# Kernel tuning notes

Measured on AMD Instinct MI355X. Metric: run time of the kernel, lower is better.

## Reference

```python
import jax, jax.numpy as jnp
import numpy as np

C = 1024
HEADS = 8
HD = C // HEADS
SF = 2
EPS = 1e-6
N, D, H, W = 2, 32, 40, 32


def _ln(x, w, b):
    m = jnp.mean(x, -1, keepdims=True)
    v = jnp.mean((x - m) ** 2, -1, keepdims=True)
    return (x - m) * jax.lax.rsqrt(v + EPS) * w + b


def _mlp2(x, w1, b1, w2, b2):
    # Linear -> exact GELU -> Linear (matches nn.Sequential(Linear, GELU, Linear))
    return jax.nn.gelu(x @ w1.T + b1, approximate=False) @ w2.T + b2


def setup_inputs() -> dict:
    key = jax.random.key(0)
    ks = jax.random.split(key, 24)
    p = lambda i, shape: jax.random.normal(ks[i], shape, jnp.float32) * 0.02
    return {
        "x": jax.random.normal(ks[0], (N, D, H, W, C), jnp.float32),
        "q_w": p(1, (C, C)),
        "k_w1": p(2, (C, C)), "k_b1": p(3, (C,)),
        "k_w2": p(4, (C, C)), "k_b2": p(5, (C,)),
        "v_w1": p(6, (C, C)), "v_b1": p(7, (C,)),
        "v_w2": p(8, (C, C)), "v_b2": p(9, (C,)),
        "lnq_w": jnp.ones((C,), jnp.float32), "lnq_b": jnp.zeros((C,), jnp.float32),
        "lnk_w": jnp.ones((C,), jnp.float32), "lnk_b": jnp.zeros((C,), jnp.float32),
        "lnv_w": jnp.ones((C,), jnp.float32), "lnv_b": jnp.zeros((C,), jnp.float32),
        "in_w": p(10, (3 * C, C)), "in_b": p(11, (3 * C,)),
        "out_w": p(12, (C, C)), "out_b": p(13, (C,)),
        "mlp_w1": p(14, (2 * C, C)), "mlp_b1": p(15, (2 * C,)),
        "mlp_w2": p(16, (2 * C, 2 * C)), "mlp_b2": p(17, (2 * C,)),
    }


def reference(x, q_w, k_w1, k_b1, k_w2, k_b2, v_w1, v_b1, v_w2, v_b2,
              lnq_w, lnq_b, lnk_w, lnk_b, lnv_w, lnv_b,
              in_w, in_b, out_w, out_b, mlp_w1, mlp_b1, mlp_w2, mlp_b2):
    n, d, h, w, c = x.shape
    dg, hg, wg = d // SF, h // SF, w // SF
    cube = SF ** 3

    x_flat = x.reshape(n, -1, c)                      # [N, T, C], T = D*H*W
    k = _ln(_mlp2(x_flat, k_w1, k_b1, k_w2, k_b2), lnk_w, lnk_b)
    v = _ln(_mlp2(x_flat, v_w1, v_b1, v_w2, v_b2), lnv_w, lnv_b)

    # Trilinear downsample by exactly 2 (align_corners=False) == 2x2x2 mean pool.
    q = x.reshape(n, dg, SF, hg, SF, wg, SF, c).mean(axis=(2, 4, 6))
    q = q.reshape(n, -1, c)                            # [N, Q, C]
    query = _ln(q @ q_w.T, lnq_w, lnq_b)               # q_proj_1 has no bias

    def regions(t):
        t = t.reshape(n, dg, SF, hg, SF, wg, SF, c)
        t = t.transpose(0, 1, 3, 5, 2, 4, 6, 7)
        return t.reshape(n, dg * hg * wg, cube, c)     # [N, Q, 8, C]

    k_r = regions(k)
    v_r = regions(v)

    wq, wk, wv = in_w[:C], in_w[C:2 * C], in_w[2 * C:]
    bq, bk, bv = in_b[:C], in_b[C:2 * C], in_b[2 * C:]
    qh = (query @ wq.T + bq).reshape(n, -1, HEADS, HD)           # [N,Q,h,hd]
    kh = (k_r @ wk.T + bk).reshape(n, -1, cube, HEADS, HD)       # [N,Q,8,h,hd]
    vh = (v_r @ wv.T + bv).reshape(n, -1, cube, HEADS, HD)

    scale = 1.0 / np.sqrt(HD).astype(np.float32)
    scores = jnp.einsum('nqhd,nqkhd->nqhk', qh, kh) * scale
    attn = jax.nn.softmax(scores, axis=-1)
    o = jnp.einsum('nqhk,nqkhd->nqhd', attn, vh).reshape(n, -1, c)
    o = o @ out_w.T + out_b                            # MHA out_proj

    o = _mlp2(o, mlp_w1, mlp_b1, mlp_w2, mlp_b2)       # [N, Q, 2C]
    return o.reshape(n, dg, hg, wg, 2 * c)
```

## Files before the change

kernel.cpp:

```cpp
#include <hip/hip_runtime.h>

typedef __attribute__((ext_vector_type(8))) short bf16x8;
typedef __attribute__((ext_vector_type(4))) float f32x4;
typedef unsigned short u16;

__device__ inline u16 f2b(float f) {
  union { float f; unsigned u; } x; x.f = f;
  unsigned r = x.u + 0x7FFFu + ((x.u >> 16) & 1u);
  return (u16)(r >> 16);
}
__device__ inline float b2f(u16 s) {
  union { unsigned u; float f; } x; x.u = ((unsigned)s) << 16;
  return x.f;
}
__device__ inline float gelu_f(float v) {
  return 0.5f * v * (1.0f + erff(v * 0.70710678118654752f));
}
__device__ inline void gll16(const void* g, void* lds) {
  __builtin_amdgcn_global_load_lds((const __attribute__((address_space(1))) void*)g,
                                   (__attribute__((address_space(3))) void*)lds,
                                   16, 0, 0);
}

__global__ __launch_bounds__(256) void cvt_w(const float* __restrict__ s,
                                             u16* __restrict__ d, int n4) {
  int i = blockIdx.x * 256 + threadIdx.x;
  if (i < n4) {
    float4 v = ((const float4*)s)[i];
    ushort4 o; o.x = f2b(v.x); o.y = f2b(v.y); o.z = f2b(v.z); o.w = f2b(v.w);
    ((ushort4*)d)[i] = o;
  }
}

__global__ __launch_bounds__(256) void pool_cvt(const float* __restrict__ xg,
                                                u16* __restrict__ Xb,
                                                u16* __restrict__ Qp) {
  int qr = blockIdx.x;
  int wgi = qr & 15;
  int hgi = (qr >> 4) % 20;
  int dgi = qr / 320;
  int c = threadIdx.x * 4;
  float sx = 0.f, sy = 0.f, sz = 0.f, sw = 0.f;
#pragma unroll
  for (int j = 0; j < 8; ++j) {
    int tr = ((2 * dgi + (j >> 2)) * 40 + (2 * hgi + ((j >> 1) & 1))) * 32 +
             (2 * wgi + (j & 1));
    long off = (long)tr * 1024 + c;
    float4 v = *(const float4*)&xg[off];
    ushort4 o; o.x = f2b(v.x); o.y = f2b(v.y); o.z = f2b(v.z); o.w = f2b(v.w);
    *(ushort4*)&Xb[off] = o;
    sx += v.x; sy += v.y; sz += v.z; sw += v.w;
  }
  ushort4 o;
  o.x = f2b(sx * 0.125f); o.y = f2b(sy * 0.125f);
  o.z = f2b(sz * 0.125f); o.w = f2b(sw * 0.125f);
  *(ushort4*)&Qp[(long)qr * 1024 + c] = o;
}

__global__ __launch_bounds__(256) void ln_ip(u16* __restrict__ X,
                                             const float* __restrict__ w,
                                             const float* __restrict__ b) {
  long row = blockIdx.x;
  int c = threadIdx.x * 4;
  ushort4 v = *(const ushort4*)&X[row * 1024 + c];
  float f0 = b2f(v.x), f1 = b2f(v.y), f2 = b2f(v.z), f3 = b2f(v.w);
  float s = f0 + f1 + f2 + f3;
  float q = f0 * f0 + f1 * f1 + f2 * f2 + f3 * f3;
#pragma unroll
  for (int off = 32; off >= 1; off >>= 1) {
    s += __shfl_xor(s, off);
    q += __shfl_xor(q, off);
  }
  __shared__ float red[8];
  int wv = threadIdx.x >> 6, ln = threadIdx.x & 63;
  if (ln == 0) { red[wv] = s; red[4 + wv] = q; }
  __syncthreads();
  s = red[0] + red[1] + red[2] + red[3];
  q = red[4] + red[5] + red[6] + red[7];
  float mean = s * (1.f / 1024.f);
  float var = q * (1.f / 1024.f) - mean * mean;
  float rs = rsqrtf(var + 1e-6f);
  float4 wv4 = *(const float4*)&w[c];
  float4 bv4 = *(const float4*)&b[c];
  ushort4 o;
  o.x = f2b((f0 - mean) * rs * wv4.x + bv4.x);
  o.y = f2b((f1 - mean) * rs * wv4.y + bv4.y);
  o.z = f2b((f2 - mean) * rs * wv4.z + bv4.z);
  o.w = f2b((f3 - mean) * rs * wv4.w + bv4.w);
  *(ushort4*)&X[row * 1024 + c] = o;
}

#define TM 128
#define TN 128
#define TK 32
template <int EPI>
__global__ __launch_bounds__(256) void gemm_bt(const u16* __restrict__ A,
                                               const u16* __restrict__ B,
                                               const float* __restrict__ bias,
                                               float* __restrict__ Cf,
                                               u16* __restrict__ Cb,
                                               int M, int N, int K) {
  __shared__ __align__(16) u16 As[TM * TK];
  __shared__ __align__(16) u16 Bs[TN * TK];
  const int tid = threadIdx.x;
  const int l = tid & 63;
  const int wv = tid >> 6;
  const int wm = (wv >> 1) * 64, wn = (wv & 1) * 64;
  const int bm = blockIdx.x * TM, bn = blockIdx.y * TN;
  const int lr = l & 15, kg = l >> 4;

  f32x4 acc[4][4] = {};

  for (int k0 = 0; k0 < K; k0 += TK) {
#pragma unroll
    for (int i = 0; i < 2; ++i) {
      int e = (i * 256 + tid) * 8;
      int r = e >> 5, c = e & 31;
      int ga = bm + r; if (ga > M - 1) ga = M - 1;
      gll16(A + (long)ga * K + k0 + c, As + e);
      int gb = bn + r;
      gll16(B + (long)gb * K + k0 + c, Bs + e);
    }
    __syncthreads();
    bf16x8 af[4], bfr[4];
#pragma unroll
    for (int m = 0; m < 4; ++m)
      af[m] = *(const bf16x8*)&As[(wm + m * 16 + lr) * TK + kg * 8];
#pragma unroll
    for (int n = 0; n < 4; ++n)
      bfr[n] = *(const bf16x8*)&Bs[(wn + n * 16 + lr) * TK + kg * 8];
#pragma unroll
    for (int m = 0; m < 4; ++m)
#pragma unroll
      for (int n = 0; n < 4; ++n)
        acc[m][n] = __builtin_amdgcn_mfma_f32_16x16x32_bf16(af[m], bfr[n],
                                                            acc[m][n], 0, 0, 0);
    __syncthreads();
  }

#pragma unroll
  for (int m = 0; m < 4; ++m) {
    int row0 = bm + wm + m * 16 + kg * 4;
#pragma unroll
    for (int n = 0; n < 4; ++n) {
      int col = bn + wn + n * 16 + lr;
      float bsv = (EPI == 3) ? 0.f : bias[col];
#pragma unroll
      for (int r = 0; r < 4; ++r) {
        int row = row0 + r;
        if (row < M) {
          float v = acc[m][n][r] + bsv;
          if (EPI == 1) v = gelu_f(v);
          if (EPI == 2) Cf[(long)row * N + col] = v;
          else Cb[(long)row * N + col] = f2b(v);
        }
      }
    }
  }
}

__global__ __launch_bounds__(256) void attn_k(const u16* __restrict__ QH,
                                              const u16* __restrict__ KH,
                                              const u16* __restrict__ VH,
                                              u16* __restrict__ O, int dgc) {
  int qr = blockIdx.x;
  int wgi = qr & 15;
  int hgi = (qr >> 4) % 20;
  int dgi = qr / 320;
  int c0 = (threadIdx.x >> 5) * 128 + (threadIdx.x & 31) * 4;
  ushort4 qv = *(const ushort4*)&QH[(long)qr * 1024 + c0];
  float q0 = b2f(qv.x), q1 = b2f(qv.y), q2 = b2f(qv.z), q3 = b2f(qv.w);
  long trs[8];
  float sc[8];
#pragma unroll
  for (int j = 0; j < 8; ++j) {
    int tr = ((2 * dgi + (j >> 2)) * 40 + (2 * hgi + ((j >> 1) & 1))) * 32 +
             (2 * wgi + (j & 1));
    trs[j] = (long)tr * 1024 + c0;
    ushort4 kv = *(const ushort4*)&KH[trs[j]];
    float p = q0 * b2f(kv.x) + q1 * b2f(kv.y) + q2 * b2f(kv.z) + q3 * b2f(kv.w);
    p += __shfl_xor(p, 16); p += __shfl_xor(p, 8); p += __shfl_xor(p, 4);
    p += __shfl_xor(p, 2);  p += __shfl_xor(p, 1);
    sc[j] = p * 0.088388347648318447f;
  }
  float mx = sc[0];
#pragma unroll
  for (int j = 1; j < 8; ++j) mx = fmaxf(mx, sc[j]);
  float ssum = 0.f;
#pragma unroll
  for (int j = 0; j < 8; ++j) { sc[j] = expf(sc[j] - mx); ssum += sc[j]; }
  float inv = 1.0f / ssum;
  float o0 = 0, o1 = 0, o2 = 0, o3 = 0;
#pragma unroll
  for (int j = 0; j < 8; ++j) {
    ushort4 vv = *(const ushort4*)&VH[trs[j]];
    float p = sc[j] * inv;
    o0 += p * b2f(vv.x); o1 += p * b2f(vv.y);
    o2 += p * b2f(vv.z); o3 += p * b2f(vv.w);
  }
  ushort4 ov; ov.x = f2b(o0); ov.y = f2b(o1); ov.z = f2b(o2); ov.w = f2b(o3);
  *(ushort4*)&O[(long)qr * 1024 + c0] = ov;
}

extern "C" void kernel_launch(void* const* d_in, const int* in_sizes, int n_in,
                              void* d_out, int out_size, void* d_ws,
                              size_t ws_size, hipStream_t stream) {
  const float* x      = (const float*)d_in[0];
  const float* q_w    = (const float*)d_in[1];
  const float* k_w1   = (const float*)d_in[2];
  const float* k_b1   = (const float*)d_in[3];
  const float* k_w2   = (const float*)d_in[4];
  const float* k_b2   = (const float*)d_in[5];
  const float* v_w1   = (const float*)d_in[6];
  const float* v_b1   = (const float*)d_in[7];
  const float* v_w2   = (const float*)d_in[8];
  const float* v_b2   = (const float*)d_in[9];
  const float* lnq_w  = (const float*)d_in[10];
  const float* lnq_b  = (const float*)d_in[11];
  const float* lnk_w  = (const float*)d_in[12];
  const float* lnk_b  = (const float*)d_in[13];
  const float* lnv_w  = (const float*)d_in[14];
  const float* lnv_b  = (const float*)d_in[15];
  const float* in_w   = (const float*)d_in[16];
  const float* in_b   = (const float*)d_in[17];
  const float* out_w  = (const float*)d_in[18];
  const float* out_b  = (const float*)d_in[19];
  const float* mlp_w1 = (const float*)d_in[20];
  const float* mlp_b1 = (const float*)d_in[21];
  const float* mlp_w2 = (const float*)d_in[22];
  const float* mlp_b2 = (const float*)d_in[23];
  float* out = (float*)d_out;

  char* base = (char*)d_ws;
  size_t off = 0;
  auto alloc_us = [&](size_t elems) -> u16* {
    u16* r = (u16*)(base + off);
    off += ((elems * 2 + 255) & ~(size_t)255);
    return r;
  };
  const size_t CC = 1024 * 1024;
  u16* wb_q   = alloc_us(CC);
  u16* wb_k1  = alloc_us(CC);
  u16* wb_k2  = alloc_us(CC);
  u16* wb_v1  = alloc_us(CC);
  u16* wb_v2  = alloc_us(CC);
  u16* wb_in  = alloc_us(3 * CC);
  u16* wb_out = alloc_us(CC);
  u16* wb_m1  = alloc_us(2 * CC);
  u16* wb_m2  = alloc_us(4 * CC);

  auto cvt = [&](const float* s, u16* d, size_t n) {
    int n4 = (int)(n / 4);
    cvt_w<<<(n4 + 255) / 256, 256, 0, stream>>>(s, d, n4);
  };
  cvt(q_w, wb_q, CC);     cvt(k_w1, wb_k1, CC);  cvt(k_w2, wb_k2, CC);
  cvt(v_w1, wb_v1, CC);   cvt(v_w2, wb_v2, CC);  cvt(in_w, wb_in, 3 * CC);
  cvt(out_w, wb_out, CC); cvt(mlp_w1, wb_m1, 2 * CC); cvt(mlp_w2, wb_m2, 4 * CC);

  int s = 16;
  for (int cand = 1; cand <= 16; cand <<= 1) {
    size_t Tc_ = 40960ull / cand;
    size_t need = off + Tc_ * 9472ull + (1ull << 20);
    if (need <= ws_size) { s = cand; break; }
  }
  const int dcount = 32 / s;
  const int dgc = dcount / 2;
  const int Tc = dcount * 1280;
  const int Tq = dgc * 320;

  u16* Xb  = alloc_us((size_t)Tc * 1024);
  u16* Hb  = alloc_us((size_t)Tc * 1024);
  u16* Kb  = alloc_us((size_t)Tc * 1024);
  u16* Vb  = alloc_us((size_t)Tc * 1024);
  u16* Qp  = alloc_us((size_t)Tq * 1024);
  u16* QQ  = alloc_us((size_t)Tq * 1024);
  u16* QHb = alloc_us((size_t)Tq * 1024);
  u16* Ob  = alloc_us((size_t)Tq * 1024);
  u16* O2  = alloc_us((size_t)Tq * 1024);
  u16* Hm  = Xb;

  dim3 gBig((Tc + 127) / 128, 1024 / 128);
  dim3 gSm((Tq + 127) / 128, 1024 / 128);
  dim3 gM1((Tq + 127) / 128, 2048 / 128);

  for (int n = 0; n < 2; ++n) {
    for (int sl = 0; sl < s; ++sl) {
      long tok0 = (long)n * 40960 + (long)sl * dcount * 1280;
      long q0g  = (long)n * 5120 + (long)sl * dgc * 320;
      const float* xg = x + tok0 * 1024;

      pool_cvt<<<Tq, 256, 0, stream>>>(xg, Xb, Qp);

      gemm_bt<1><<<gBig, 256, 0, stream>>>(Xb, wb_k1, k_b1, nullptr, Hb, Tc, 1024, 1024);
      gemm_bt<0><<<gBig, 256, 0, stream>>>(Hb, wb_k2, k_b2, nullptr, Kb, Tc, 1024, 1024);
      ln_ip<<<Tc, 256, 0, stream>>>(Kb, lnk_w, lnk_b);

      gemm_bt<1><<<gBig, 256, 0, stream>>>(Xb, wb_v1, v_b1, nullptr, Hb, Tc, 1024, 1024);
      gemm_bt<0><<<gBig, 256, 0, stream>>>(Hb, wb_v2, v_b2, nullptr, Vb, Tc, 1024, 1024);
      ln_ip<<<Tc, 256, 0, stream>>>(Vb, lnv_w, lnv_b);

      gemm_bt<3><<<gSm, 256, 0, stream>>>(Qp, wb_q, nullptr, nullptr, QQ, Tq, 1024, 1024);
      ln_ip<<<Tq, 256, 0, stream>>>(QQ, lnq_w, lnq_b);
      gemm_bt<0><<<gSm, 256, 0, stream>>>(QQ, wb_in, in_b, nullptr, QHb, Tq, 1024, 1024);

      gemm_bt<0><<<gBig, 256, 0, stream>>>(Kb, wb_in + CC, in_b + 1024, nullptr, Hb, Tc, 1024, 1024);
      gemm_bt<0><<<gBig, 256, 0, stream>>>(Vb, wb_in + 2 * CC, in_b + 2048, nullptr, Xb, Tc, 1024, 1024);

      attn_k<<<Tq, 256, 0, stream>>>(QHb, Hb, Xb, Ob, dgc);

      gemm_bt<0><<<gSm, 256, 0, stream>>>(Ob, wb_out, out_b, nullptr, O2, Tq, 1024, 1024);
      gemm_bt<1><<<gM1, 256, 0, stream>>>(O2, wb_m1, mlp_b1, nullptr, Hm, Tq, 2048, 1024);
      gemm_bt<2><<<gM1, 256, 0, stream>>>(Hm, wb_m2, mlp_b2, out + q0g * 2048, nullptr, Tq, 2048, 2048);
    }
  }
}
```

Baseline: 2.686 ms.

## Double-buffer GEMM LDS tiles, fuse K/V first MLP layers, add XCD-aware block swizzle

The GEMM kernel now uses two LDS buffers so the next K-tile loads while the current one is computed, halving the number of barriers per tile. The K and V first MLP layers are merged into one N=2048 GEMM over concatenated weights and biases, and the second layers read strided halves through a new lda parameter. Blocks are launched on a 1D grid and remapped so each XCD gets contiguous M-tiles, meant to improve L2 reuse. The trade-off is double the LDS per block, which may lower occupancy, plus a larger hidden buffer that can force more slices.

Measured after the change: 2.314 ms. 1.16x faster.

```diff
diff --git a/kernel.cpp b/kernel.cpp
--- a/kernel.cpp
+++ b/kernel.cpp
@@ -30,6 +30,13 @@
     ushort4 o; o.x = f2b(v.x); o.y = f2b(v.y); o.z = f2b(v.z); o.w = f2b(v.w);
     ((ushort4*)d)[i] = o;
   }
+}
+
+__global__ __launch_bounds__(256) void cat_bias(const float* __restrict__ a,
+                                                const float* __restrict__ b,
+                                                float* __restrict__ o) {
+  int i = blockIdx.x * 256 + threadIdx.x;
+  if (i < 1024) { o[i] = a[i]; o[1024 + i] = b[i]; }
 }
 
 __global__ __launch_bounds__(256) void pool_cvt(const float* __restrict__ xg,
@@ -90,53 +97,83 @@
   *(ushort4*)&X[row * 1024 + c] = o;
 }
 
-#define TM 128
-#define TN 128
-#define TK 32
+#define BK 32
 template <int EPI>
 __global__ __launch_bounds__(256) void gemm_bt(const u16* __restrict__ A,
                                                const u16* __restrict__ B,
                                                const float* __restrict__ bias,
                                                float* __restrict__ Cf,
                                                u16* __restrict__ Cb,
-                                               int M, int N, int K) {
-  __shared__ __align__(16) u16 As[TM * TK];
-  __shared__ __align__(16) u16 Bs[TN * TK];
+                                               int M, int N, int K, int lda,
+                                               int nbx, int nby) {
+  __shared__ __align__(16) u16 As0[128 * BK];
+  __shared__ __align__(16) u16 Bs0[128 * BK];
+  __shared__ __align__(16) u16 As1[128 * BK];
+  __shared__ __align__(16) u16 Bs1[128 * BK];
   const int tid = threadIdx.x;
-  const int l = tid & 63;
-  const int wv = tid >> 6;
+
+  int L = blockIdx.x, bx, by;
+  if ((nbx & 7) == 0) {
+    int xcd = L & 7, j = L >> 3, ppx = nbx >> 3;
+    int pj = j / nby;
+    bx = xcd * ppx + pj;
+    by = j - pj * nby;
+  } else {
+    bx = L % nbx;
+    by = L / nbx;
+  }
+  const int bm = bx * 128, bn = by * 128;
+
+  const int l = tid & 63, wv = tid >> 6;
   const int wm = (wv >> 1) * 64, wn = (wv & 1) * 64;
-  const int bm = blockIdx.x * TM, bn = blockIdx.y * TN;
   const int lr = l & 15, kg = l >> 4;
 
+  const int ea = tid * 8, eb = (256 + tid) * 8;
+  const int ra = ea >> 5, ca = ea & 31;
+  const int rb = eb >> 5, cbn = eb & 31;
+  int gra = bm + ra; if (gra > M - 1) gra = M - 1;
+  int grb = bm + rb; if (grb > M - 1) grb = M - 1;
+  const u16* pa0 = A + (long)gra * lda + ca;
+  const u16* pa1 = A + (long)grb * lda + cbn;
+  const u16* pb0 = B + (long)(bn + ra) * K + ca;
+  const u16* pb1 = B + (long)(bn + rb) * K + cbn;
+
   f32x4 acc[4][4] = {};
-
-  for (int k0 = 0; k0 < K; k0 += TK) {
-#pragma unroll
-    for (int i = 0; i < 2; ++i) {
-      int e = (i * 256 + tid) * 8;
-      int r = e >> 5, c = e & 31;
-      int ga = bm + r; if (ga > M - 1) ga = M - 1;
-      gll16(A + (long)ga * K + k0 + c, As + e);
-      int gb = bn + r;
-      gll16(B + (long)gb * K + k0 + c, Bs + e);
-    }
+  const int nt = K / BK;
+
+#define STAGE(AS, BS, k0)                \
+  do {                                   \
+    gll16(pa0 + (k0), &(AS)[ea]);        \
+    gll16(pb0 + (k0), &(BS)[ea]);        \
+    gll16(pa1 + (k0), &(AS)[eb]);        \
+    gll16(pb1 + (k0), &(BS)[eb]);        \
+  } while (0)
+
+#define COMPUTE(AS, BS)                                                       \
+  do {                                                                        \
+    bf16x8 af[4], bfr[4];                                                     \
+    _Pragma("unroll") for (int m = 0; m < 4; ++m)                             \
+        af[m] = *(const bf16x8*)&(AS)[(wm + m * 16 + lr) * BK + kg * 8];      \
+    _Pragma("unroll") for (int n = 0; n < 4; ++n)                             \
+        bfr[n] = *(const bf16x8*)&(BS)[(wn + n * 16 + lr) * BK + kg * 8];     \
+    _Pragma("unroll") for (int m = 0; m < 4; ++m)                             \
+        _Pragma("unroll") for (int n = 0; n < 4; ++n)                         \
+            acc[m][n] = __builtin_amdgcn_mfma_f32_16x16x32_bf16(              \
+                af[m], bfr[n], acc[m][n], 0, 0, 0);                           \
+  } while (0)
+
+  STAGE(As0, Bs0, 0);
+  __syncthreads();
+  for (int t = 0; t < nt; t += 2) {
+    if (t + 1 < nt) STAGE(As1, Bs1, (t + 1) * BK);
+    COMPUTE(As0, Bs0);
     __syncthreads();
-    bf16x8 af[4], bfr[4];
-#pragma unroll
-    for (int m = 0; m < 4; ++m)
-      af[m] = *(const bf16x8*)&As[(wm + m * 16 + lr) * TK + kg * 8];
-#pragma unroll
-    for (int n = 0; n < 4; ++n)
-      bfr[n] = *(const bf16x8*)&Bs[(wn + n * 16 + lr) * TK + kg * 8];
-#pragma unroll
-    for (int m = 0; m < 4; ++m)
-#pragma unroll
-      for (int n = 0; n < 4; ++n)
-        acc[m][n] = __builtin_amdgcn_mfma_f32_16x16x32_bf16(af[m], bfr[n],
-                                                            acc[m][n], 0, 0, 0);
+    if (t + 2 < nt) STAGE(As0, Bs0, (t + 2) * BK);
+    COMPUTE(As1, Bs1);
     __syncthreads();
   }
+#undef STAGE
+#undef COMPUTE
 
 #pragma unroll
   for (int m = 0; m < 4; ++m) {
@@ -162,7 +199,7 @@
 __global__ __launch_bounds__(256) void attn_k(const u16* __restrict__ QH,
                                               const u16* __restrict__ KH,
                                               const u16* __restrict__ VH,
-                                              u16* __restrict__ O, int dgc) {
+                                              u16* __restrict__ O) {
   int qr = blockIdx.x;
   int wgi = qr & 15;
   int hgi = (qr >> 4) % 20;
@@ -240,27 +277,30 @@
   };
   const size_t CC = 1024 * 1024;
   u16* wb_q   = alloc_us(CC);
-  u16* wb_k1  = alloc_us(CC);
+  u16* wb_kv1 = alloc_us(2 * CC);
   u16* wb_k2  = alloc_us(CC);
-  u16* wb_v1  = alloc_us(CC);
   u16* wb_v2  = alloc_us(CC);
   u16* wb_in  = alloc_us(3 * CC);
   u16* wb_out = alloc_us(CC);
   u16* wb_m1  = alloc_us(2 * CC);
   u16* wb_m2  = alloc_us(4 * CC);
+  float* b_kv1 = (float*)(base + off); off += 2048 * 4;
 
   auto cvt = [&](const float* s, u16* d, size_t n) {
     int n4 = (int)(n / 4);
     cvt_w<<<(n4 + 255) / 256, 256, 0, stream>>>(s, d, n4);
   };
-  cvt(q_w, wb_q, CC);     cvt(k_w1, wb_k1, CC);  cvt(k_w2, wb_k2, CC);
-  cvt(v_w1, wb_v1, CC);   cvt(v_w2, wb_v2, CC);  cvt(in_w, wb_in, 3 * CC);
-  cvt(out_w, wb_out, CC); cvt(mlp_w1, wb_m1, 2 * CC); cvt(mlp_w2, wb_m2, 4 * CC);
+  cvt(q_w, wb_q, CC);
+  cvt(k_w1, wb_kv1, CC);        cvt(v_w1, wb_kv1 + CC, CC);
+  cvt(k_w2, wb_k2, CC);         cvt(v_w2, wb_v2, CC);
+  cvt(in_w, wb_in, 3 * CC);     cvt(out_w, wb_out, CC);
+  cvt(mlp_w1, wb_m1, 2 * CC);   cvt(mlp_w2, wb_m2, 4 * CC);
+  cat_bias<<<4, 256, 0, stream>>>(k_b1, v_b1, b_kv1);
 
   int s = 16;
   for (int cand = 1; cand <= 16; cand <<= 1) {
     size_t Tc_ = 40960ull / cand;
-    size_t need = off + Tc_ * 9472ull + (1ull << 20);
+    size_t need = off + Tc_ * 11520ull + (1ull << 20);
     if (need <= ws_size) { s = cand; break; }
   }
   const int dcount = 32 / s;
@@ -269,7 +309,7 @@
   const int Tq = dgc * 320;
 
   u16* Xb  = alloc_us((size_t)Tc * 1024);
-  u16* Hb  = alloc_us((size_t)Tc * 1024);
+  u16* Hb2 = alloc_us((size_t)Tc * 2048);
   u16* Kb  = alloc_us((size_t)Tc * 1024);
   u16* Vb  = alloc_us((size_t)Tc * 1024);
   u16* Qp  = alloc_us((size_t)Tq * 1024);
@@ -277,11 +317,19 @@
   u16* QHb = alloc_us((size_t)Tq * 1024);
   u16* Ob  = alloc_us((size_t)Tq * 1024);
   u16* O2  = alloc_us((size_t)Tq * 1024);
-  u16* Hm  = Xb;
-
-  dim3 gBig((Tc + 127) / 128, 1024 / 128);
-  dim3 gSm((Tq + 127) / 128, 1024 / 128);
-  dim3 gM1((Tq + 127) / 128, 2048 / 128);
+  u16* Hm  = Kb;
+
+  auto launch_gemm = [&](int EPI, const u16* A, const u16* B, const float* bias,
+                         float* Cf, u16* Cb, int M, int N, int K, int lda) {
+    int nbx = (M + 127) / 128, nby = N / 128;
+    dim3 g(nbx * nby);
+    switch (EPI) {
+      case 0: gemm_bt<0><<<g, 256, 0, stream>>>(A, B, bias, Cf, Cb, M, N, K, lda, nbx, nby); break;
+      case 1: gemm_bt<1><<<g, 256, 0, stream>>>(A, B, bias, Cf, Cb, M, N, K, lda, nbx, nby); break;
+      case 2: gemm_bt<2><<<g, 256, 0, stream>>>(A, B, bias, Cf, Cb, M, N, K, lda, nbx, nby); break;
+      default: gemm_bt<3><<<g, 256, 0, stream>>>(A, B, bias, Cf, Cb, M, N, K, lda, nbx, nby); break;
+    }
+  };
 
   for (int n = 0; n < 2; ++n) {
     for (int sl = 0; sl < s; ++sl) {
@@ -291,26 +339,24 @@
 
       pool_cvt<<<Tq, 256, 0, stream>>>(xg, Xb, Qp);
 
-      gemm_bt<1><<<gBig, 256, 0, stream>>>(Xb, wb_k1, k_b1, nullptr, Hb, Tc, 1024, 1024);
-      gemm_bt<0><<<gBig, 256, 0, stream>>>(Hb, wb_k2, k_b2, nullptr, Kb, Tc, 1024, 1024);
+      launch_gemm(1, Xb, wb_kv1, b_kv1, nullptr, Hb2, Tc, 2048, 1024, 1024);
+      launch_gemm(0, Hb2, wb_k2, k_b2, nullptr, Kb, Tc, 1024, 1024, 2048);
       ln_ip<<<Tc, 256, 0, stream>>>(Kb, lnk_w, lnk_b);
-
-      gemm_bt<1><<<gBig, 256, 0, stream>>>(Xb, wb_v1, v_b1, nullptr, Hb, Tc, 1024, 1024);
-      gemm_bt<0><<<gBig, 256, 0, stream>>>(Hb, wb_v2, v_b2, nullptr, Vb, Tc, 1024, 1024);
+      launch_gemm(0, Hb2 + 1024, wb_v2, v_b2, nullptr, Vb, Tc, 1024, 1024, 2048);
       ln_ip<<<Tc, 256, 0, stream>>>(Vb, lnv_w, lnv_b);
 
-      gemm_bt<3><<<gSm, 256, 0, stream>>>(Qp, wb_q, nullptr, nullptr, QQ, Tq, 1024, 1024);
+      launch_gemm(3, Qp, wb_q, nullptr, nullptr, QQ, Tq, 1024, 1024, 1024);
       ln_ip<<<Tq, 256, 0, stream>>>(QQ, lnq_w, lnq_b);
-      gemm_bt<0><<<gSm, 256, 0, stream>>>(QQ, wb_in, in_b, nullptr, QHb, Tq, 1024, 1024);
-
-      gemm_bt<0><<<gBig, 256, 0, stream>>>(Kb, wb_in + CC, in_b + 1024, nullptr, Hb, Tc, 1024, 1024);
-      gemm_bt<0><<<gBig, 256, 0, stream>>>(Vb, wb_in + 2 * CC, in_b + 2048, nullptr, Xb, Tc, 1024, 1024);
-
-      attn_k<<<Tq, 256, 0, stream>>>(QHb, Hb, Xb, Ob, dgc);
-
-      gemm_bt<0><<<gSm, 256, 0, stream>>>(Ob, wb_out, out_b, nullptr, O2, Tq, 1024, 1024);
-      gemm_bt<1><<<gM1, 256, 0, stream>>>(O2, wb_m1, mlp_b1, nullptr, Hm, Tq, 2048, 1024);
-      gemm_bt<2><<<gM1, 256, 0, stream>>>(Hm, wb_m2, mlp_b2, out + q0g * 2048, nullptr, Tq, 2048, 2048);
+      launch_gemm(0, QQ, wb_in, in_b, nullptr, QHb, Tq, 1024, 1024, 1024);
+
+      launch_gemm(0, Kb, wb_in + CC, in_b + 1024, nullptr, Xb, Tc, 1024, 1024, 1024);
+      launch_gemm(0, Vb, wb_in + 2 * CC, in_b + 2048, nullptr, Hb2, Tc, 1024, 1024, 1024);
+
+      attn_k<<<Tq, 256, 0, stream>>>(QHb, Xb, Hb2, Ob);
+
+      launch_gemm(0, Ob, wb_out, out_b, nullptr, O2, Tq, 1024, 1024, 1024);
+      launch_gemm(1, O2, wb_m1, mlp_b1, nullptr, Hm, Tq, 2048, 1024, 1024);
+      launch_gemm(2, Hm, wb_m2, mlp_b2, out + q0g * 2048, nullptr, Tq, 2048, 2048, 2048);
     }
   }
 }
```
